# Kernel optimization log

Hardware: AMD Instinct MI355X
Metric: run time of the kernel (lower is better)

## Reference

```python
import jax, jax.numpy as jnp
import numpy as np

EMBED = 768
HEADS = 12
HEAD_DIM = EMBED // HEADS


def setup_inputs() -> dict:
    key = jax.random.key(0)
    ks = jax.random.split(key, 7)
    B, S = 4, 2048
    scale = 1.0 / np.sqrt(EMBED)
    return {
        "q": jax.random.normal(ks[0], (B, S, EMBED), dtype=jnp.float32),
        "k": jax.random.normal(ks[1], (B, S, EMBED), dtype=jnp.float32),
        "v": jax.random.normal(ks[2], (B, S, EMBED), dtype=jnp.float32),
        # NOTE: original torch code applies self.query to q, k AND v (bug kept faithfully),
        # so only the query projection and the output projection participate.
        "Wq": (jax.random.normal(ks[3], (EMBED, EMBED), dtype=jnp.float32) * scale),
        "bq": jnp.zeros((EMBED,), dtype=jnp.float32),
        "Wo": (jax.random.normal(ks[4], (EMBED, EMBED), dtype=jnp.float32) * scale),
        "bo": jnp.zeros((EMBED,), dtype=jnp.float32),
    }


def _split_heads(x):
    B, S, _ = x.shape
    return x.reshape(B, S, HEADS, HEAD_DIM).transpose(0, 2, 1, 3)  # [B,H,S,D]


def reference(q, k, v, Wq, bq, Wo, bo):
    # All three streams go through the *query* projection (faithful to source bug).
    qh = _split_heads(q @ Wq.T + bq)
    kh = _split_heads(k @ Wq.T + bq)
    vh = _split_heads(v @ Wq.T + bq)
    scores = jnp.einsum("bhsd,bhtd->bhst", qh, kh) / np.sqrt(HEAD_DIM)  # [B,H,S,S]
    attn = jax.nn.softmax(scores, axis=-1)  # dropout = identity (eval mode)
    out = jnp.einsum("bhst,bhtd->bhsd", attn, vh)  # [B,H,S,D]
    B, H, S, D = out.shape
    out = out.transpose(0, 2, 1, 3).reshape(B, S, H * D)  # [B,S,E]
    return out @ Wo.T + bo
```

## Files before the change

### kernel.cpp

```cpp
#include <hip/hip_runtime.h>

typedef unsigned int  uint32;
typedef unsigned short ushort_t;

using s16x8 = __attribute__((ext_vector_type(8))) short;
using bf8v  = __attribute__((ext_vector_type(8))) __bf16;
using f16x4 = __attribute__((ext_vector_type(4))) _Float16;
using f16x8 = __attribute__((ext_vector_type(8))) _Float16;
using f32x4 = __attribute__((ext_vector_type(4))) float;

typedef __attribute__((address_space(1))) void as1_void;
typedef __attribute__((address_space(3))) void as3_void;

__device__ __forceinline__ void gld16(const void* g, void* l) {
  __builtin_amdgcn_global_load_lds((const as1_void*)g, (as3_void*)l, 16, 0, 0);
}

__device__ __forceinline__ f32x4 mfma32(s16x8 a, s16x8 b, f32x4 c) {
  return __builtin_amdgcn_mfma_f32_16x16x32_bf16(
      __builtin_bit_cast(bf8v, a), __builtin_bit_cast(bf8v, b), c, 0, 0, 0);
}
__device__ __forceinline__ f32x4 mfma32h(f16x8 a, f16x8 b, f32x4 c) {
  return __builtin_amdgcn_mfma_f32_16x16x32_f16(a, b, c, 0, 0, 0);
}

__device__ __forceinline__ ushort_t f2bf(float f) {
  uint32 u = __float_as_uint(f);
  u += 0x7FFFu + ((u >> 16) & 1u);
  return (ushort_t)(u >> 16);
}
__device__ __forceinline__ f16x4 exp_pack(f32x4 st, float CS, float FM) {
  float e0 = __builtin_amdgcn_exp2f(__builtin_fmaf(st[0], CS, -FM));
  float e1 = __builtin_amdgcn_exp2f(__builtin_fmaf(st[1], CS, -FM));
  float e2 = __builtin_amdgcn_exp2f(__builtin_fmaf(st[2], CS, -FM));
  float e3 = __builtin_amdgcn_exp2f(__builtin_fmaf(st[3], CS, -FM));
  uint2 u = {__builtin_bit_cast(uint32, __builtin_amdgcn_cvt_pkrtz(e0, e1)),
             __builtin_bit_cast(uint32, __builtin_amdgcn_cvt_pkrtz(e2, e3))};
  return __builtin_bit_cast(f16x4, u);
}

__global__ __launch_bounds__(256) void cvt_all(const float* __restrict__ q,
                                               const float* __restrict__ k,
                                               const float* __restrict__ v,
                                               const float* __restrict__ Wq,
                                               const float* __restrict__ Wo,
                                               ushort_t* qb, ushort_t* kb, ushort_t* vb,
                                               ushort_t* wqb, ushort_t* wob) {
  int i = blockIdx.x * 256 + threadIdx.x;
  const float* s; ushort_t* d; int off;
  if (i < 4718592) {
    int st = i / 1572864; off = i - st * 1572864;
    s = st == 0 ? q : (st == 1 ? k : v);
    d = st == 0 ? qb : (st == 1 ? kb : vb);
  } else {
    int j = i - 4718592; int st = j / 147456; off = j - st * 147456;
    s = st ? Wo : Wq; d = st ? wob : wqb;
  }
  float4 f = ((const float4*)s)[off];
  ushort4 o = {f2bf(f.x), f2bf(f.y), f2bf(f.z), f2bf(f.w)};
  ((ushort4*)d)[off] = o;
}

__device__ __forceinline__ void gemm_core(const ushort_t* __restrict__ A,
                                          const ushort_t* __restrict__ Bw,
                                          ushort_t* As, ushort_t* Bs,
                                          int m0, int n0, f32x4 (&acc)[4][4]) {
  const int tid = threadIdx.x;
  const int wave = tid >> 6, lane = tid & 63;
  const int qd = lane >> 4, c = lane & 15;
  const int wm = wave >> 1, wn = wave & 1;
  const int pc0 = qd ^ (c & 7), pc1 = (4 + qd) ^ (c & 7);
  int row[4], cl[4], lb[4];
#pragma unroll
  for (int i = 0; i < 4; ++i) {
    int s = i * 256 + wave * 64 + lane;
    row[i] = s >> 3; cl[i] = (s & 7) ^ (row[i] & 7);
    lb[i] = (i * 256 + wave * 64) * 16;
  }
  for (int kt = 0; kt < 12; ++kt) {
    __syncthreads();
#pragma unroll
    for (int i = 0; i < 4; ++i) {
      gld16(A + (size_t)(m0 + row[i]) * 768 + kt * 64 + cl[i] * 8, (char*)As + lb[i]);
      gld16(Bw + (size_t)(n0 + row[i]) * 768 + kt * 64 + cl[i] * 8, (char*)Bs + lb[i]);
    }
    __syncthreads();
#pragma unroll
    for (int kk = 0; kk < 2; ++kk) {
      const int pcr = kk ? pc1 : pc0;
      s16x8 a[4], b[4];
#pragma unroll
      for (int i = 0; i < 4; ++i) a[i] = *(const s16x8*)(As + (wm * 64 + i * 16 + c) * 64 + pcr * 8);
#pragma unroll
      for (int j = 0; j < 4; ++j) b[j] = *(const s16x8*)(Bs + (wn * 64 + j * 16 + c) * 64 + pcr * 8);
#pragma unroll
      for (int i = 0; i < 4; ++i)
#pragma unroll
        for (int j = 0; j < 4; ++j) acc[i][j] = mfma32(a[i], b[j], acc[i][j]);
    }
  }
}

__global__ __launch_bounds__(256) void gemm_proj(const ushort_t* __restrict__ qb,
                                                 const ushort_t* __restrict__ kb,
                                                 const ushort_t* __restrict__ vb,
                                                 const ushort_t* __restrict__ Wqb,
                                                 const float* __restrict__ bias,
                                                 ushort_t* __restrict__ qh,
                                                 ushort_t* __restrict__ kh,
                                                 ushort_t* __restrict__ vt) {
  __shared__ __align__(16) ushort_t As[8192];
  __shared__ __align__(16) ushort_t Bs[8192];
  const int bz = blockIdx.z;
  const ushort_t* A = bz == 0 ? qb : (bz == 1 ? kb : vb);
  const int m0 = blockIdx.y * 128, n0 = blockIdx.x * 128;
  f32x4 acc[4][4] = {};
  gemm_core(A, Wqb, As, Bs, m0, n0, acc);
  const int tid = threadIdx.x, wave = tid >> 6, lane = tid & 63;
  const int qd = lane >> 4, c = lane & 15;
  const int wm = wave >> 1, wn = wave & 1;
  if (bz == 2) {
    const int sbase = m0 & 2047, bb = m0 >> 11;
#pragma unroll
    for (int p = 0; p < 2; ++p) {
      __syncthreads();
      if (wn == p) {
#pragma unroll
        for (int j = 0; j < 4; ++j) {
          int n64 = j * 16 + c;
          float bv = bias[n0 + p * 64 + n64];
#pragma unroll
          for (int i = 0; i < 4; ++i) {
            int ps8 = (wm * 16 + i * 4 + qd) ^ ((c & 7) << 2);
            uint2 w = {__builtin_bit_cast(uint32, __builtin_amdgcn_cvt_pkrtz(acc[i][j][0] + bv, acc[i][j][1] + bv)),
                       __builtin_bit_cast(uint32, __builtin_amdgcn_cvt_pkrtz(acc[i][j][2] + bv, acc[i][j][3] + bv))};
            *(uint2*)(As + n64 * 128 + ps8 * 4) = w;
          }
        }
      }
      __syncthreads();
      const int h = (n0 >> 6) + p;
#pragma unroll
      for (int e = 0; e < 4; ++e) {
        int ch = e * 256 + tid;
        int n64 = ch >> 4, u = ch & 15;
        uint4 w = *(const uint4*)(As + n64 * 128 + (u ^ ((n64 & 7) << 1)) * 8);
        *(uint4*)(vt + ((size_t)(bb * 12 + h) * 64 + n64) * 2048 + sbase + u * 8) = w;
      }
    }
  } else {
    ushort_t* dst = bz == 0 ? qh : kh;
#pragma unroll
    for (int j = 0; j < 4; ++j) {
      int n = n0 + wn * 64 + j * 16 + c;
      float bv = bias[n];
      int h = n >> 6, d = n & 63;
#pragma unroll
      for (int i = 0; i < 4; ++i)
#pragma unroll
        for (int r = 0; r < 4; ++r) {
          int m = m0 + wm * 64 + i * 16 + qd * 4 + r;
          int bb = m >> 11, s = m & 2047;
          dst[((size_t)((bb * 12 + h) * 2048 + s)) * 64 + d] = f2bf(acc[i][j][r] + bv);
        }
    }
  }
}

__global__ __launch_bounds__(256) void gemm_final(const ushort_t* __restrict__ A,
                                                  const ushort_t* __restrict__ Wob,
                                                  const float* __restrict__ bias,
                                                  float* __restrict__ out) {
  __shared__ __align__(16) ushort_t As[8192];
  __shared__ __align__(16) ushort_t Bs[8192];
  const int m0 = blockIdx.y * 128, n0 = blockIdx.x * 128;
  f32x4 acc[4][4] = {};
  gemm_core(A, Wob, As, Bs, m0, n0, acc);
  const int tid = threadIdx.x, wave = tid >> 6, lane = tid & 63;
  const int qd = lane >> 4, c = lane & 15;
  const int wm = wave >> 1, wn = wave & 1;
#pragma unroll
  for (int j = 0; j < 4; ++j) {
    int n = n0 + wn * 64 + j * 16 + c;
    float bv = bias[n];
#pragma unroll
    for (int i = 0; i < 4; ++i)
#pragma unroll
      for (int r = 0; r < 4; ++r) {
        int m = m0 + wm * 64 + i * 16 + qd * 4 + r;
        out[(size_t)m * 768 + n] = acc[i][j][r] + bv;
      }
  }
}

__global__ __launch_bounds__(256, 3) void flash(const ushort_t* __restrict__ qh,
                                                const ushort_t* __restrict__ kh,
                                                const ushort_t* __restrict__ vt,
                                                ushort_t* __restrict__ attn) {
  __shared__ __align__(16) ushort_t Ks[128 * 64];
  __shared__ __align__(16) ushort_t Vts[64 * 128];
  const int bid = blockIdx.x;
  const int bh = bid % 48, qt = bid / 48;
  const int tid = threadIdx.x, wave = tid >> 6, lane = tid & 63;
  const int qd = lane >> 4, c = lane & 15;
  const ushort_t* Qg = qh + (size_t)bh * 131072;
  const ushort_t* Kg = kh + (size_t)bh * 131072;
  const ushort_t* Vg = vt + (size_t)bh * 131072;
  const int sb = qt * 128 + wave * 32;

  s16x8 qf[2][2];
#pragma unroll
  for (int ts = 0; ts < 2; ++ts)
#pragma unroll
    for (int kk = 0; kk < 2; ++kk)
      qf[ts][kk] = *(const s16x8*)(Qg + (size_t)(sb + ts * 16 + c) * 64 + kk * 32 + qd * 8);

  const f32x4 z4 = {0.f, 0.f, 0.f, 0.f};
  f32x4 o[2][4], lacc[2];
#pragma unroll
  for (int ts = 0; ts < 2; ++ts) {
    lacc[ts] = z4;
#pragma unroll
    for (int dn = 0; dn < 4; ++dn) o[ts][dn] = z4;
  }
  f16x8 ones8;
#pragma unroll
  for (int e = 0; e < 8; ++e) ones8[e] = (_Float16)1.f;
  const float CS = 0.125f * 1.4426950408889634f;
  const float FM = 12.0f;

  const int kpc0 = (qd) ^ (c & 7);
  const int kpc1 = (4 + qd) ^ (c & 7);

  int kgrow[4], kcl[4], vrow[4], vcl[4], lbase[4];
#pragma unroll
  for (int i = 0; i < 4; ++i) {
    int s = i * 256 + wave * 64 + lane;
    int kr = s >> 3; kcl[i] = (s & 7) ^ (kr & 7);
    int u = kr & 31;
    kgrow[i] = (kr & ~31) | (((u >> 2) & 3) << 3) | (((u >> 4) & 1) << 2) | (u & 3);
    vrow[i] = s >> 4; vcl[i] = (s & 15) ^ (vrow[i] & 15);
    lbase[i] = (i * 256 + wave * 64) * 16;
  }

  for (int kt = 0; kt < 16; ++kt) {
    __syncthreads();
#pragma unroll
    for (int i = 0; i < 4; ++i)
      gld16(Kg + (size_t)(kt * 128 + kgrow[i]) * 64 + kcl[i] * 8, (char*)Ks + lbase[i]);
#pragma unroll
    for (int i = 0; i < 4; ++i)
      gld16(Vg + (size_t)vrow[i] * 2048 + kt * 128 + vcl[i] * 8, (char*)Vts + lbase[i]);
    __syncthreads();

#pragma unroll
    for (int p = 0; p < 4; ++p) {
      f16x4 p0[2], p1[2];
#pragma unroll
      for (int tile = 0; tile < 2; ++tile) {
        const int r = (p * 2 + tile) * 16 + c;
        s16x8 a0 = *(const s16x8*)(Ks + r * 64 + kpc0 * 8);
        s16x8 a1 = *(const s16x8*)(Ks + r * 64 + kpc1 * 8);
        f32x4 st0 = mfma32(a0, qf[0][0], z4);
        f32x4 st1 = mfma32(a0, qf[1][0], z4);
        st0 = mfma32(a1, qf[0][1], st0);
        st1 = mfma32(a1, qf[1][1], st1);
        p0[tile] = exp_pack(st0, CS, FM);
        p1[tile] = exp_pack(st1, CS, FM);
      }
      f16x8 A0 = __builtin_shufflevector(p0[0], p0[1], 0, 1, 2, 3, 4, 5, 6, 7);
      f16x8 A1 = __builtin_shufflevector(p1[0], p1[1], 0, 1, 2, 3, 4, 5, 6, 7);
      lacc[0] = mfma32h(A0, ones8, lacc[0]);
      lacc[1] = mfma32h(A1, ones8, lacc[1]);
#pragma unroll
      for (int dn = 0; dn < 4; ++dn) {
        f16x8 vb = *(const f16x8*)(Vts + (dn * 16 + c) * 128 + ((4 * p + qd) ^ c) * 8);
        o[0][dn] = mfma32h(A0, vb, o[0][dn]);
        o[1][dn] = mfma32h(A1, vb, o[1][dn]);
      }
    }
  }

  const int bb = bh / 12, h = bh % 12;
#pragma unroll
  for (int ts = 0; ts < 2; ++ts)
#pragma unroll
    for (int r = 0; r < 4; ++r) {
      float inv = 1.f / lacc[ts][r];
      int s = sb + ts * 16 + qd * 4 + r;
#pragma unroll
      for (int dn = 0; dn < 4; ++dn) {
        float val = o[ts][dn][r] * inv;
        attn[((size_t)(bb * 2048 + s)) * 768 + h * 64 + dn * 16 + c] = f2bf(val);
      }
    }
}

extern "C" void kernel_launch(void* const* d_in, const int* in_sizes, int n_in,
                              void* d_out, int out_size, void* d_ws, size_t ws_size,
                              hipStream_t stream) {
  const float* q  = (const float*)d_in[0];
  const float* k  = (const float*)d_in[1];
  const float* v  = (const float*)d_in[2];
  const float* Wq = (const float*)d_in[3];
  const float* bq = (const float*)d_in[4];
  const float* Wo = (const float*)d_in[5];
  const float* bo = (const float*)d_in[6];
  float* out = (float*)d_out;
  char* ws = (char*)d_ws;

  ushort_t* qbf = (ushort_t*)(ws + 0);
  ushort_t* kbf = (ushort_t*)(ws + 12582912);
  ushort_t* vbf = (ushort_t*)(ws + 25165824);
  ushort_t* wqb = (ushort_t*)(ws + 37748736);
  ushort_t* wob = (ushort_t*)(ws + 38928384);
  ushort_t* qhp = (ushort_t*)(ws + 40108032);
  ushort_t* khp = (ushort_t*)(ws + 52690944);
  ushort_t* vtp = (ushort_t*)(ws + 65273856);
  ushort_t* att = (ushort_t*)(ws + 0);

  cvt_all<<<dim3(19584), 256, 0, stream>>>(q, k, v, Wq, Wo, qbf, kbf, vbf, wqb, wob);
  gemm_proj<<<dim3(6, 64, 3), 256, 0, stream>>>(qbf, kbf, vbf, wqb, bq, qhp, khp, vtp);
  flash<<<dim3(768), 256, 0, stream>>>(qhp, khp, vtp, att);
  gemm_final<<<dim3(6, 64), 256, 0, stream>>>(att, wob, bo, out);
}
```

Measured before the change: 252.5 us.

## Prefetch next K/V tile into registers and fold softmax scale into Q

The attention loop now loads the next K and V tile into registers while the current tile is being computed, then writes them to LDS after the compute. This replaces the blocking load-then-barrier pattern. The softmax scale is applied in the Q projection epilogue, and the constant max offset is used as the MFMA accumulator init, so the per-element FMA before exp2 goes away. s_setprio hints are added to favor waves issuing MFMAs. The cost is extra registers for the prefetch buffers and slightly different rounding of the scaled Q values.

```diff
diff --git a/kernel.cpp b/kernel.cpp
--- a/kernel.cpp
+++ b/kernel.cpp
@@ -29,11 +29,11 @@
   u += 0x7FFFu + ((u >> 16) & 1u);
   return (ushort_t)(u >> 16);
 }
-__device__ __forceinline__ f16x4 exp_pack(f32x4 st, float CS, float FM) {
-  float e0 = __builtin_amdgcn_exp2f(__builtin_fmaf(st[0], CS, -FM));
-  float e1 = __builtin_amdgcn_exp2f(__builtin_fmaf(st[1], CS, -FM));
-  float e2 = __builtin_amdgcn_exp2f(__builtin_fmaf(st[2], CS, -FM));
-  float e3 = __builtin_amdgcn_exp2f(__builtin_fmaf(st[3], CS, -FM));
+__device__ __forceinline__ f16x4 exp_pack(f32x4 st) {
+  float e0 = __builtin_amdgcn_exp2f(st[0]);
+  float e1 = __builtin_amdgcn_exp2f(st[1]);
+  float e2 = __builtin_amdgcn_exp2f(st[2]);
+  float e3 = __builtin_amdgcn_exp2f(st[3]);
   uint2 u = {__builtin_bit_cast(uint32, __builtin_amdgcn_cvt_pkrtz(e0, e1)),
              __builtin_bit_cast(uint32, __builtin_amdgcn_cvt_pkrtz(e2, e3))};
   return __builtin_bit_cast(f16x4, u);
@@ -150,6 +150,7 @@
     }
   } else {
     ushort_t* dst = bz == 0 ? qh : kh;
+    const float qsc = bz == 0 ? 0.18033688011112042f : 1.0f;
 #pragma unroll
     for (int j = 0; j < 4; ++j) {
       int n = n0 + wn * 64 + j * 16 + c;
@@ -161,7 +162,7 @@
         for (int r = 0; r < 4; ++r) {
           int m = m0 + wm * 64 + i * 16 + qd * 4 + r;
           int bb = m >> 11, s = m & 2047;
-          dst[((size_t)((bb * 12 + h) * 2048 + s)) * 64 + d] = f2bf(acc[i][j][r] + bv);
+          dst[((size_t)((bb * 12 + h) * 2048 + s)) * 64 + d] = f2bf((acc[i][j][r] + bv) * qsc);
         }
     }
   }
@@ -216,6 +217,8 @@
       qf[ts][kk] = *(const s16x8*)(Qg + (size_t)(sb + ts * 16 + c) * 64 + kk * 32 + qd * 8);
 
   const f32x4 z4 = {0.f, 0.f, 0.f, 0.f};
+  const float FM = 12.0f;
+  const f32x4 nFM = {-FM, -FM, -FM, -FM};
   f32x4 o[2][4], lacc[2];
 #pragma unroll
   for (int ts = 0; ts < 2; ++ts) {
@@ -226,8 +229,6 @@
   f16x8 ones8;
 #pragma unroll
   for (int e = 0; e < 8; ++e) ones8[e] = (_Float16)1.f;
-  const float CS = 0.125f * 1.4426950408889634f;
-  const float FM = 12.0f;
 
   const int kpc0 = (qd) ^ (c & 7);
   const int kpc1 = (4 + qd) ^ (c & 7);
@@ -243,15 +244,24 @@
     lbase[i] = (i * 256 + wave * 64) * 16;
   }
 
+#pragma unroll
+  for (int i = 0; i < 4; ++i)
+    gld16(Kg + (size_t)kgrow[i] * 64 + kcl[i] * 8, (char*)Ks + lbase[i]);
+#pragma unroll
+  for (int i = 0; i < 4; ++i)
+    gld16(Vg + (size_t)vrow[i] * 2048 + vcl[i] * 8, (char*)Vts + lbase[i]);
+  __syncthreads();
+
   for (int kt = 0; kt < 16; ++kt) {
-    __syncthreads();
-#pragma unroll
-    for (int i = 0; i < 4; ++i)
-      gld16(Kg + (size_t)(kt * 128 + kgrow[i]) * 64 + kcl[i] * 8, (char*)Ks + lbase[i]);
-#pragma unroll
-    for (int i = 0; i < 4; ++i)
-      gld16(Vg + (size_t)vrow[i] * 2048 + kt * 128 + vcl[i] * 8, (char*)Vts + lbase[i]);
-    __syncthreads();
+    uint4 kpre[4], vpre[4];
+    if (kt < 15) {
+#pragma unroll
+      for (int i = 0; i < 4; ++i)
+        kpre[i] = *(const uint4*)(Kg + (size_t)((kt + 1) * 128 + kgrow[i]) * 64 + kcl[i] * 8);
+#pragma unroll
+      for (int i = 0; i < 4; ++i)
+        vpre[i] = *(const uint4*)(Vg + (size_t)vrow[i] * 2048 + (kt + 1) * 128 + vcl[i] * 8);
+    }
 
 #pragma unroll
     for (int p = 0; p < 4; ++p) {
@@ -261,15 +271,18 @@
         const int r = (p * 2 + tile) * 16 + c;
         s16x8 a0 = *(const s16x8*)(Ks + r * 64 + kpc0 * 8);
         s16x8 a1 = *(const s16x8*)(Ks + r * 64 + kpc1 * 8);
-        f32x4 st0 = mfma32(a0, qf[0][0], z4);
-        f32x4 st1 = mfma32(a0, qf[1][0], z4);
+        __builtin_amdgcn_s_setprio(1);
+        f32x4 st0 = mfma32(a0, qf[0][0], nFM);
+        f32x4 st1 = mfma32(a0, qf[1][0], nFM);
         st0 = mfma32(a1, qf[0][1], st0);
         st1 = mfma32(a1, qf[1][1], st1);
-        p0[tile] = exp_pack(st0, CS, FM);
-        p1[tile] = exp_pack(st1, CS, FM);
+        __builtin_amdgcn_s_setprio(0);
+        p0[tile] = exp_pack(st0);
+        p1[tile] = exp_pack(st1);
       }
       f16x8 A0 = __builtin_shufflevector(p0[0], p0[1], 0, 1, 2, 3, 4, 5, 6, 7);
       f16x8 A1 = __builtin_shufflevector(p1[0], p1[1], 0, 1, 2, 3, 4, 5, 6, 7);
+      __builtin_amdgcn_s_setprio(1);
       lacc[0] = mfma32h(A0, ones8, lacc[0]);
       lacc[1] = mfma32h(A1, ones8, lacc[1]);
 #pragma unroll
@@ -278,6 +291,18 @@
         o[0][dn] = mfma32h(A0, vb, o[0][dn]);
         o[1][dn] = mfma32h(A1, vb, o[1][dn]);
       }
+      __builtin_amdgcn_s_setprio(0);
+    }
+
+    if (kt < 15) {
+      __syncthreads();
+#pragma unroll
+      for (int i = 0; i < 4; ++i)
+        *(uint4*)((char*)Ks + lbase[i] + lane * 16) = kpre[i];
+#pragma unroll
+      for (int i = 0; i < 4; ++i)
+        *(uint4*)((char*)Vts + lbase[i] + lane * 16) = vpre[i];
+      __syncthreads();
     }
   }
 
```

New measurement: 317.3 us. 1.26x slower.

## Halve flash query tile, fold softmax scale into Q projection, add MFMA priority

Applied to the files above, without the earlier changes.

The flash kernel now handles 64 queries per block (16 per wave) instead of 128, doubling the grid to 1536 blocks and raising the occupancy hint to 5 blocks per CU. The softmax scale (1/8 × log2 e) is folded into the Q projection epilogue, and the -FM offset is passed as the MFMA accumulator init, so the per-element FMA before exp2 goes away. s_setprio is placed around the MFMA sections to help interleave waves. The trade-off is that each K/V tile loaded into LDS is now reused by half as many queries, which doubles K/V traffic, and Q gains an extra bf16 rounding step after scaling.

```diff
diff --git a/kernel.cpp b/kernel.cpp
--- a/kernel.cpp
+++ b/kernel.cpp
@@ -29,11 +29,11 @@
   u += 0x7FFFu + ((u >> 16) & 1u);
   return (ushort_t)(u >> 16);
 }
-__device__ __forceinline__ f16x4 exp_pack(f32x4 st, float CS, float FM) {
-  float e0 = __builtin_amdgcn_exp2f(__builtin_fmaf(st[0], CS, -FM));
-  float e1 = __builtin_amdgcn_exp2f(__builtin_fmaf(st[1], CS, -FM));
-  float e2 = __builtin_amdgcn_exp2f(__builtin_fmaf(st[2], CS, -FM));
-  float e3 = __builtin_amdgcn_exp2f(__builtin_fmaf(st[3], CS, -FM));
+__device__ __forceinline__ f16x4 exp_pack(f32x4 st) {
+  float e0 = __builtin_amdgcn_exp2f(st[0]);
+  float e1 = __builtin_amdgcn_exp2f(st[1]);
+  float e2 = __builtin_amdgcn_exp2f(st[2]);
+  float e3 = __builtin_amdgcn_exp2f(st[3]);
   uint2 u = {__builtin_bit_cast(uint32, __builtin_amdgcn_cvt_pkrtz(e0, e1)),
              __builtin_bit_cast(uint32, __builtin_amdgcn_cvt_pkrtz(e2, e3))};
   return __builtin_bit_cast(f16x4, u);
@@ -150,6 +150,7 @@
     }
   } else {
     ushort_t* dst = bz == 0 ? qh : kh;
+    const float qsc = bz == 0 ? 0.18033688011112042f : 1.0f;
 #pragma unroll
     for (int j = 0; j < 4; ++j) {
       int n = n0 + wn * 64 + j * 16 + c;
@@ -161,7 +162,7 @@
         for (int r = 0; r < 4; ++r) {
           int m = m0 + wm * 64 + i * 16 + qd * 4 + r;
           int bb = m >> 11, s = m & 2047;
-          dst[((size_t)((bb * 12 + h) * 2048 + s)) * 64 + d] = f2bf(acc[i][j][r] + bv);
+          dst[((size_t)((bb * 12 + h) * 2048 + s)) * 64 + d] = f2bf((acc[i][j][r] + bv) * qsc);
         }
     }
   }
@@ -193,7 +194,7 @@
   }
 }
 
-__global__ __launch_bounds__(256, 3) void flash(const ushort_t* __restrict__ qh,
+__global__ __launch_bounds__(256, 5) void flash(const ushort_t* __restrict__ qh,
                                                 const ushort_t* __restrict__ kh,
                                                 const ushort_t* __restrict__ vt,
                                                 ushort_t* __restrict__ attn) {
@@ -206,28 +207,22 @@
   const ushort_t* Qg = qh + (size_t)bh * 131072;
   const ushort_t* Kg = kh + (size_t)bh * 131072;
   const ushort_t* Vg = vt + (size_t)bh * 131072;
-  const int sb = qt * 128 + wave * 32;
-
-  s16x8 qf[2][2];
-#pragma unroll
-  for (int ts = 0; ts < 2; ++ts)
-#pragma unroll
-    for (int kk = 0; kk < 2; ++kk)
-      qf[ts][kk] = *(const s16x8*)(Qg + (size_t)(sb + ts * 16 + c) * 64 + kk * 32 + qd * 8);
+  const int sb = qt * 64 + wave * 16;
+
+  s16x8 qf[2];
+#pragma unroll
+  for (int kk = 0; kk < 2; ++kk)
+    qf[kk] = *(const s16x8*)(Qg + (size_t)(sb + c) * 64 + kk * 32 + qd * 8);
 
   const f32x4 z4 = {0.f, 0.f, 0.f, 0.f};
-  f32x4 o[2][4], lacc[2];
-#pragma unroll
-  for (int ts = 0; ts < 2; ++ts) {
-    lacc[ts] = z4;
-#pragma unroll
-    for (int dn = 0; dn < 4; ++dn) o[ts][dn] = z4;
-  }
+  const float FM = 12.0f;
+  const f32x4 nFM = {-FM, -FM, -FM, -FM};
+  f32x4 o[4], lacc = z4;
+#pragma unroll
+  for (int dn = 0; dn < 4; ++dn) o[dn] = z4;
   f16x8 ones8;
 #pragma unroll
   for (int e = 0; e < 8; ++e) ones8[e] = (_Float16)1.f;
-  const float CS = 0.125f * 1.4426950408889634f;
-  const float FM = 12.0f;
 
   const int kpc0 = (qd) ^ (c & 7);
   const int kpc1 = (4 + qd) ^ (c & 7);
@@ -255,45 +250,41 @@
 
 #pragma unroll
     for (int p = 0; p < 4; ++p) {
-      f16x4 p0[2], p1[2];
+      f16x4 p0[2];
 #pragma unroll
       for (int tile = 0; tile < 2; ++tile) {
         const int r = (p * 2 + tile) * 16 + c;
         s16x8 a0 = *(const s16x8*)(Ks + r * 64 + kpc0 * 8);
         s16x8 a1 = *(const s16x8*)(Ks + r * 64 + kpc1 * 8);
-        f32x4 st0 = mfma32(a0, qf[0][0], z4);
-        f32x4 st1 = mfma32(a0, qf[1][0], z4);
-        st0 = mfma32(a1, qf[0][1], st0);
-        st1 = mfma32(a1, qf[1][1], st1);
-        p0[tile] = exp_pack(st0, CS, FM);
-        p1[tile] = exp_pack(st1, CS, FM);
+        __builtin_amdgcn_s_setprio(1);
+        f32x4 st0 = mfma32(a0, qf[0], nFM);
+        st0 = mfma32(a1, qf[1], st0);
+        __builtin_amdgcn_s_setprio(0);
+        p0[tile] = exp_pack(st0);
       }
       f16x8 A0 = __builtin_shufflevector(p0[0], p0[1], 0, 1, 2, 3, 4, 5, 6, 7);
-      f16x8 A1 = __builtin_shufflevector(p1[0], p1[1], 0, 1, 2, 3, 4, 5, 6, 7);
-      lacc[0] = mfma32h(A0, ones8, lacc[0]);
-      lacc[1] = mfma32h(A1, ones8, lacc[1]);
+      __builtin_amdgcn_s_setprio(1);
+      lacc = mfma32h(A0, ones8, lacc);
 #pragma unroll
       for (int dn = 0; dn < 4; ++dn) {
         f16x8 vb = *(const f16x8*)(Vts + (dn * 16 + c) * 128 + ((4 * p + qd) ^ c) * 8);
-        o[0][dn] = mfma32h(A0, vb, o[0][dn]);
-        o[1][dn] = mfma32h(A1, vb, o[1][dn]);
-      }
+        o[dn] = mfma32h(A0, vb, o[dn]);
+      }
+      __builtin_amdgcn_s_setprio(0);
     }
   }
 
   const int bb = bh / 12, h = bh % 12;
 #pragma unroll
-  for (int ts = 0; ts < 2; ++ts)
-#pragma unroll
-    for (int r = 0; r < 4; ++r) {
-      float inv = 1.f / lacc[ts][r];
-      int s = sb + ts * 16 + qd * 4 + r;
-#pragma unroll
-      for (int dn = 0; dn < 4; ++dn) {
-        float val = o[ts][dn][r] * inv;
-        attn[((size_t)(bb * 2048 + s)) * 768 + h * 64 + dn * 16 + c] = f2bf(val);
-      }
-    }
+  for (int r = 0; r < 4; ++r) {
+    float inv = 1.f / lacc[r];
+    int s = sb + qd * 4 + r;
+#pragma unroll
+    for (int dn = 0; dn < 4; ++dn) {
+      float val = o[dn][r] * inv;
+      attn[((size_t)(bb * 2048 + s)) * 768 + h * 64 + dn * 16 + c] = f2bf(val);
+    }
+  }
 }
 
 extern "C" void kernel_launch(void* const* d_in, const int* in_sizes, int n_in,
@@ -321,6 +312,6 @@
 
   cvt_all<<<dim3(19584), 256, 0, stream>>>(q, k, v, Wq, Wo, qbf, kbf, vbf, wqb, wob);
   gemm_proj<<<dim3(6, 64, 3), 256, 0, stream>>>(qbf, kbf, vbf, wqb, bq, qhp, khp, vtp);
-  flash<<<dim3(768), 256, 0, stream>>>(qhp, khp, vtp, att);
+  flash<<<dim3(1536), 256, 0, stream>>>(qhp, khp, vtp, att);
   gemm_final<<<dim3(6, 64), 256, 0, stream>>>(att, wob, bo, out);
 }
```

Result: slower. 258.4 us (+2.3%).
